# Kernel tuning notes

Hardware: AMD Instinct MI355X
Metric: run time of the kernel (lower is better)

## Reference

```python
import jax, jax.numpy as jnp
import numpy as np

IN_F, OUT_F, RANK, BLK = 4096, 4096, 64, 64
N_BLOCKS = min(IN_F, OUT_F) // BLK  # 64


def setup_inputs() -> dict:
    key = jax.random.key(0)
    ks = jax.random.split(key, 6)
    s = 0.02
    x = jax.random.normal(ks[0], (4, 2048, IN_F), dtype=jnp.float32)
    diag_params = jax.random.normal(ks[1], (N_BLOCKS, IN_F // N_BLOCKS, OUT_F // N_BLOCKS), dtype=jnp.float32) * s
    W_left = jax.random.normal(ks[2], (RANK, IN_F), dtype=jnp.float32) * s   # torch Linear weight [out,in]
    W_right = jax.random.normal(ks[3], (OUT_F, RANK), dtype=jnp.float32) * s
    b_right = jax.random.normal(ks[4], (OUT_F,), dtype=jnp.float32) * s
    bias = jax.random.normal(ks[5], (OUT_F,), dtype=jnp.float32) * s
    return {"x": x, "diag_params": diag_params, "W_left": W_left,
            "W_right": W_right, "b_right": b_right, "bias": bias}


def reference(x, diag_params, W_left, W_right, b_right, bias):
    nb, bi, bo = diag_params.shape
    lead = x.shape[:-1]
    # block-diagonal matmul: x @ block_diag(*diag_params), without materializing the dense matrix
    xb = x.reshape(*lead, nb, bi)                       # [..., nb, bi]
    x1 = jnp.einsum('...nd,ndo->...no', xb, diag_params).reshape(*lead, nb * bo)
    # low-rank path: right(left(x)) with right's bias
    x2 = (x @ W_left.T) @ W_right.T + b_right
    return x1 + x2 + bias
```

## Files before the change

### kernel.cpp

```cpp
#include <hip/hip_runtime.h>
#include <hip/hip_bf16.h>
#include <stdint.h>


#define M_TOT   8192
#define IN_F    4096
#define OUT_F   4096
#define RANK    64
#define NBLK    64

typedef __attribute__((ext_vector_type(8))) short  bf16x8;
typedef __attribute__((ext_vector_type(4))) float  floatx4;

#define WS_BIAS   0
#define WS_WL     16384
#define WS_BP     540672
#define WS_T      1589248

__device__ __forceinline__ unsigned short f2bf(float f) {
    union { float f; unsigned int u; } v; v.f = f;
    unsigned int u = v.u;
    u += 0x7fffu + ((u >> 16) & 1u);
    return (unsigned short)(u >> 16);
}

__global__ __launch_bounds__(256) void prep_kernel(
    const float* __restrict__ diag, const float* __restrict__ Wl,
    const float* __restrict__ Wr,   const float* __restrict__ br,
    const float* __restrict__ bias,
    float* __restrict__ bias_comb, unsigned short* __restrict__ wl_pack,
    unsigned short* __restrict__ bp_pack)
{
    int tid = blockIdx.x * blockDim.x + threadIdx.x;
    int nthr = gridDim.x * blockDim.x;

    for (int i = tid; i < OUT_F; i += nthr)
        bias_comb[i] = br[i] + bias[i];

    for (int i = tid; i < 64 * 4096; i += nthr) {
        int n = i >> 12, c = i & 4095;
        wl_pack[((size_t)(c >> 5) * 64 + n) * 32 + (c & 31)] = f2bf(Wl[i]);
    }

    for (int i = tid; i < 64 * 64 * 64; i += nthr) {
        int nb = i >> 12, k = (i >> 6) & 63, n = i & 63;
        bp_pack[(((size_t)nb * 4 + (k >> 5)) * 64 + n) * 32 + (k & 31)] = f2bf(diag[i]);
    }

    for (int i = tid; i < 64 * 64 * 64; i += nthr) {
        int nb = i >> 12, n = (i >> 6) & 63, r = i & 63;
        int kt = 64 + r;
        bp_pack[(((size_t)nb * 4 + (kt >> 5)) * 64 + n) * 32 + (kt & 31)] = f2bf(Wr[i]);
    }
}

__global__ __launch_bounds__(256) void k1_lowrank(
    const float* __restrict__ x, const unsigned short* __restrict__ wl_pack,
    float* __restrict__ t)
{
    int wave = blockIdx.x * 4 + (threadIdx.x >> 6);
    int lane = threadIdx.x & 63;
    int q = lane >> 4, l = lane & 15;
    int mt = wave >> 3;
    int ks = wave & 7;
    int m0 = mt * 16;
    int kc0 = ks * 16;

    const float* xrow = x + (size_t)(m0 + l) * IN_F + q * 8;
    floatx4 acc[4] = {};

    #pragma unroll 4
    for (int kc = kc0; kc < kc0 + 16; ++kc) {
        const float* ap = xrow + kc * 32;
        float4 a0 = *(const float4*)(ap);
        float4 a1 = *(const float4*)(ap + 4);
        bf16x8 af;
        af[0] = (short)f2bf(a0.x); af[1] = (short)f2bf(a0.y);
        af[2] = (short)f2bf(a0.z); af[3] = (short)f2bf(a0.w);
        af[4] = (short)f2bf(a1.x); af[5] = (short)f2bf(a1.y);
        af[6] = (short)f2bf(a1.z); af[7] = (short)f2bf(a1.w);
        #pragma unroll
        for (int nt = 0; nt < 4; ++nt) {
            bf16x8 bf = *(const bf16x8*)(wl_pack + ((size_t)(kc * 64 + nt * 16 + l) * 32 + q * 8));
            acc[nt] = __builtin_amdgcn_mfma_f32_16x16x32_bf16(af, bf, acc[nt], 0, 0, 0);
        }
    }

    #pragma unroll
    for (int nt = 0; nt < 4; ++nt)
        #pragma unroll
        for (int r = 0; r < 4; ++r)
            atomicAdd(&t[(size_t)(m0 + q * 4 + r) * RANK + nt * 16 + l], acc[nt][r]);
}

__global__ __launch_bounds__(256) void k2_out(
    const float* __restrict__ x, const unsigned short* __restrict__ bp_pack,
    const float* __restrict__ t, const float* __restrict__ bias_comb,
    float* __restrict__ out)
{
    int wave = blockIdx.x * 4 + (threadIdx.x >> 6);
    int lane = threadIdx.x & 63;
    int nb = wave >> 7;
    int mg = wave & 127;
    int q = lane >> 4, l = lane & 15;

    bf16x8 bfrag[4][4];
    #pragma unroll
    for (int kc = 0; kc < 4; ++kc)
        #pragma unroll
        for (int nt = 0; nt < 4; ++nt)
            bfrag[kc][nt] = *(const bf16x8*)(bp_pack +
                (((size_t)(nb * 4 + kc) * 64 + nt * 16 + l) * 32 + q * 8));

    float bval[4];
    #pragma unroll
    for (int nt = 0; nt < 4; ++nt)
        bval[nt] = bias_comb[nb * 64 + nt * 16 + l];

    float4 xa[8], xn[8];
    auto load_sub = [&](int sub, float4* dst) {
        int m0 = (mg * 4 + sub) * 16;
        const float* xp = x + (size_t)(m0 + l) * IN_F + nb * 64 + q * 8;
        dst[0] = *(const float4*)(xp);
        dst[1] = *(const float4*)(xp + 4);
        dst[2] = *(const float4*)(xp + 32);
        dst[3] = *(const float4*)(xp + 36);
        const float* tp = t + (size_t)(m0 + l) * RANK + q * 8;
        dst[4] = *(const float4*)(tp);
        dst[5] = *(const float4*)(tp + 4);
        dst[6] = *(const float4*)(tp + 32);
        dst[7] = *(const float4*)(tp + 36);
    };

    load_sub(0, xa);
    for (int sub = 0; sub < 4; ++sub) {
        if (sub < 3) load_sub(sub + 1, xn);

        bf16x8 afrag[4];
        #pragma unroll
        for (int kc = 0; kc < 4; ++kc) {
            float4 a0 = xa[kc * 2], a1 = xa[kc * 2 + 1];
            bf16x8 af;
            af[0] = (short)f2bf(a0.x); af[1] = (short)f2bf(a0.y);
            af[2] = (short)f2bf(a0.z); af[3] = (short)f2bf(a0.w);
            af[4] = (short)f2bf(a1.x); af[5] = (short)f2bf(a1.y);
            af[6] = (short)f2bf(a1.z); af[7] = (short)f2bf(a1.w);
            afrag[kc] = af;
        }

        floatx4 acc[4] = {};
        #pragma unroll
        for (int kc = 0; kc < 4; ++kc)
            #pragma unroll
            for (int nt = 0; nt < 4; ++nt)
                acc[nt] = __builtin_amdgcn_mfma_f32_16x16x32_bf16(afrag[kc], bfrag[kc][nt], acc[nt], 0, 0, 0);

        int m0 = (mg * 4 + sub) * 16;
        float* op = out + (size_t)m0 * OUT_F + nb * 64;
        #pragma unroll
        for (int nt = 0; nt < 4; ++nt)
            #pragma unroll
            for (int r = 0; r < 4; ++r)
                op[(size_t)(q * 4 + r) * OUT_F + nt * 16 + l] = acc[nt][r] + bval[nt];

        #pragma unroll
        for (int i = 0; i < 8; ++i) xa[i] = xn[i];
    }
}

extern "C" void kernel_launch(void* const* d_in, const int* in_sizes, int n_in,
                              void* d_out, int out_size, void* d_ws, size_t ws_size,
                              hipStream_t stream) {
    const float* x    = (const float*)d_in[0];
    const float* diag = (const float*)d_in[1];
    const float* Wl   = (const float*)d_in[2];
    const float* Wr   = (const float*)d_in[3];
    const float* br   = (const float*)d_in[4];
    const float* bias = (const float*)d_in[5];
    float* out = (float*)d_out;

    char* ws = (char*)d_ws;
    float*          bias_comb = (float*)(ws + WS_BIAS);
    unsigned short* wl_pack   = (unsigned short*)(ws + WS_WL);
    unsigned short* bp_pack   = (unsigned short*)(ws + WS_BP);
    float*          t         = (float*)(ws + WS_T);

    hipMemsetAsync(t, 0, (size_t)M_TOT * RANK * sizeof(float), stream);

    hipLaunchKernelGGL(prep_kernel, dim3(512), dim3(256), 0, stream,
                       diag, Wl, Wr, br, bias, bias_comb, wl_pack, bp_pack);
    hipLaunchKernelGGL(k1_lowrank, dim3(1024), dim3(256), 0, stream,
                       x, wl_pack, t);
    hipLaunchKernelGGL(k2_out, dim3(2048), dim3(256), 0, stream,
                       x, bp_pack, t, bias_comb, out);
}
```

Baseline: 315.4 us.

## Fuse low-rank projection and block-diagonal output into one kernel with LDS reduction

The low-rank x@W_left pass and the output pass are merged into a single kernel. Each block owns 16 rows, keeps the converted bf16 x fragments in registers (32 per wave), and reduces the four per-wave partial t values through shared memory instead of global atomics. This removes the memset, the atomics, the t round trip through global memory and the second read of x. The cost is heavy register pressure (xfrag[32] plus B fragments), only 512 blocks, and B fragments reloaded for each of the 16 block-diagonal tiles.

```diff
diff --git a/kernel.cpp b/kernel.cpp
--- a/kernel.cpp
+++ b/kernel.cpp
@@ -15,13 +15,23 @@
 #define WS_BIAS   0
 #define WS_WL     16384
 #define WS_BP     540672
-#define WS_T      1589248
+
+#define S_TP 68
 
 __device__ __forceinline__ unsigned short f2bf(float f) {
     union { float f; unsigned int u; } v; v.f = f;
     unsigned int u = v.u;
     u += 0x7fffu + ((u >> 16) & 1u);
     return (unsigned short)(u >> 16);
+}
+
+__device__ __forceinline__ bf16x8 cvt8(float4 a0, float4 a1) {
+    bf16x8 af;
+    af[0] = (short)f2bf(a0.x); af[1] = (short)f2bf(a0.y);
+    af[2] = (short)f2bf(a0.z); af[3] = (short)f2bf(a0.w);
+    af[4] = (short)f2bf(a1.x); af[5] = (short)f2bf(a1.y);
+    af[6] = (short)f2bf(a1.z); af[7] = (short)f2bf(a1.w);
+    return af;
 }
 
 __global__ __launch_bounds__(256) void prep_kernel(
@@ -54,35 +64,37 @@
     }
 }
 
-__global__ __launch_bounds__(256) void k1_lowrank(
+__global__ __launch_bounds__(256, 2) void fused_kernel(
     const float* __restrict__ x, const unsigned short* __restrict__ wl_pack,
-    float* __restrict__ t)
+    const unsigned short* __restrict__ bp_pack, const float* __restrict__ bias_comb,
+    float* __restrict__ out)
 {
-    int wave = blockIdx.x * 4 + (threadIdx.x >> 6);
+    __shared__ float t_part[4 * 16 * S_TP];
+
+    int w = threadIdx.x >> 6;
     int lane = threadIdx.x & 63;
     int q = lane >> 4, l = lane & 15;
-    int mt = wave >> 3;
-    int ks = wave & 7;
+    int mt = blockIdx.x;
     int m0 = mt * 16;
-    int kc0 = ks * 16;
+    int kc_g0 = w * 32;
 
     const float* xrow = x + (size_t)(m0 + l) * IN_F + q * 8;
-    floatx4 acc[4] = {};
 
-    #pragma unroll 4
-    for (int kc = kc0; kc < kc0 + 16; ++kc) {
-        const float* ap = xrow + kc * 32;
+    bf16x8 xfrag[32];
+    floatx4 tacc[4] = {};
+
+    #pragma unroll
+    for (int kc = 0; kc < 32; ++kc) {
+        int kc_g = kc_g0 + kc;
+        const float* ap = xrow + kc_g * 32;
         float4 a0 = *(const float4*)(ap);
         float4 a1 = *(const float4*)(ap + 4);
-        bf16x8 af;
-        af[0] = (short)f2bf(a0.x); af[1] = (short)f2bf(a0.y);
-        af[2] = (short)f2bf(a0.z); af[3] = (short)f2bf(a0.w);
-        af[4] = (short)f2bf(a1.x); af[5] = (short)f2bf(a1.y);
-        af[6] = (short)f2bf(a1.z); af[7] = (short)f2bf(a1.w);
+        bf16x8 af = cvt8(a0, a1);
+        xfrag[kc] = af;
         #pragma unroll
         for (int nt = 0; nt < 4; ++nt) {
-            bf16x8 bf = *(const bf16x8*)(wl_pack + ((size_t)(kc * 64 + nt * 16 + l) * 32 + q * 8));
-            acc[nt] = __builtin_amdgcn_mfma_f32_16x16x32_bf16(af, bf, acc[nt], 0, 0, 0);
+            bf16x8 bf = *(const bf16x8*)(wl_pack + ((size_t)(kc_g * 64 + nt * 16 + l) * 32 + q * 8));
+            tacc[nt] = __builtin_amdgcn_mfma_f32_16x16x32_bf16(af, bf, tacc[nt], 0, 0, 0);
         }
     }
 
@@ -90,81 +102,58 @@
     for (int nt = 0; nt < 4; ++nt)
         #pragma unroll
         for (int r = 0; r < 4; ++r)
-            atomicAdd(&t[(size_t)(m0 + q * 4 + r) * RANK + nt * 16 + l], acc[nt][r]);
-}
+            t_part[w * 16 * S_TP + (q * 4 + r) * S_TP + nt * 16 + l] = tacc[nt][r];
 
-__global__ __launch_bounds__(256) void k2_out(
-    const float* __restrict__ x, const unsigned short* __restrict__ bp_pack,
-    const float* __restrict__ t, const float* __restrict__ bias_comb,
-    float* __restrict__ out)
-{
-    int wave = blockIdx.x * 4 + (threadIdx.x >> 6);
-    int lane = threadIdx.x & 63;
-    int nb = wave >> 7;
-    int mg = wave & 127;
-    int q = lane >> 4, l = lane & 15;
+    __syncthreads();
 
-    bf16x8 bfrag[4][4];
+    bf16x8 tfrag[2];
     #pragma unroll
-    for (int kc = 0; kc < 4; ++kc)
+    for (int kc2 = 0; kc2 < 2; ++kc2) {
+        float4 s0 = {0.f, 0.f, 0.f, 0.f}, s1 = {0.f, 0.f, 0.f, 0.f};
         #pragma unroll
-        for (int nt = 0; nt < 4; ++nt)
-            bfrag[kc][nt] = *(const bf16x8*)(bp_pack +
-                (((size_t)(nb * 4 + kc) * 64 + nt * 16 + l) * 32 + q * 8));
+        for (int p = 0; p < 4; ++p) {
+            const float* tp = &t_part[p * 16 * S_TP + l * S_TP + kc2 * 32 + q * 8];
+            float4 v0 = *(const float4*)(tp);
+            float4 v1 = *(const float4*)(tp + 4);
+            s0.x += v0.x; s0.y += v0.y; s0.z += v0.z; s0.w += v0.w;
+            s1.x += v1.x; s1.y += v1.y; s1.z += v1.z; s1.w += v1.w;
+        }
+        tfrag[kc2] = cvt8(s0, s1);
+    }
 
-    float bval[4];
     #pragma unroll
-    for (int nt = 0; nt < 4; ++nt)
-        bval[nt] = bias_comb[nb * 64 + nt * 16 + l];
+    for (int i = 0; i < 16; ++i) {
+        int nb = w * 16 + i;
 
-    float4 xa[8], xn[8];
-    auto load_sub = [&](int sub, float4* dst) {
-        int m0 = (mg * 4 + sub) * 16;
-        const float* xp = x + (size_t)(m0 + l) * IN_F + nb * 64 + q * 8;
-        dst[0] = *(const float4*)(xp);
-        dst[1] = *(const float4*)(xp + 4);
-        dst[2] = *(const float4*)(xp + 32);
-        dst[3] = *(const float4*)(xp + 36);
-        const float* tp = t + (size_t)(m0 + l) * RANK + q * 8;
-        dst[4] = *(const float4*)(tp);
-        dst[5] = *(const float4*)(tp + 4);
-        dst[6] = *(const float4*)(tp + 32);
-        dst[7] = *(const float4*)(tp + 36);
-    };
-
-    load_sub(0, xa);
-    for (int sub = 0; sub < 4; ++sub) {
-        if (sub < 3) load_sub(sub + 1, xn);
-
-        bf16x8 afrag[4];
-        #pragma unroll
-        for (int kc = 0; kc < 4; ++kc) {
-            float4 a0 = xa[kc * 2], a1 = xa[kc * 2 + 1];
-            bf16x8 af;
-            af[0] = (short)f2bf(a0.x); af[1] = (short)f2bf(a0.y);
-            af[2] = (short)f2bf(a0.z); af[3] = (short)f2bf(a0.w);
-            af[4] = (short)f2bf(a1.x); af[5] = (short)f2bf(a1.y);
-            af[6] = (short)f2bf(a1.z); af[7] = (short)f2bf(a1.w);
-            afrag[kc] = af;
-        }
-
-        floatx4 acc[4] = {};
+        bf16x8 bfrag[4][4];
         #pragma unroll
         for (int kc = 0; kc < 4; ++kc)
             #pragma unroll
             for (int nt = 0; nt < 4; ++nt)
-                acc[nt] = __builtin_amdgcn_mfma_f32_16x16x32_bf16(afrag[kc], bfrag[kc][nt], acc[nt], 0, 0, 0);
+                bfrag[kc][nt] = *(const bf16x8*)(bp_pack +
+                    (((size_t)(nb * 4 + kc) * 64 + nt * 16 + l) * 32 + q * 8));
 
-        int m0 = (mg * 4 + sub) * 16;
+        floatx4 acc[4];
+        #pragma unroll
+        for (int nt = 0; nt < 4; ++nt) {
+            float bv = bias_comb[nb * 64 + nt * 16 + l];
+            acc[nt][0] = bv; acc[nt][1] = bv; acc[nt][2] = bv; acc[nt][3] = bv;
+        }
+
+        #pragma unroll
+        for (int kc = 0; kc < 4; ++kc) {
+            bf16x8 af = (kc < 2) ? xfrag[2 * i + kc] : tfrag[kc - 2];
+            #pragma unroll
+            for (int nt = 0; nt < 4; ++nt)
+                acc[nt] = __builtin_amdgcn_mfma_f32_16x16x32_bf16(af, bfrag[kc][nt], acc[nt], 0, 0, 0);
+        }
+
         float* op = out + (size_t)m0 * OUT_F + nb * 64;
         #pragma unroll
         for (int nt = 0; nt < 4; ++nt)
             #pragma unroll
             for (int r = 0; r < 4; ++r)
-                op[(size_t)(q * 4 + r) * OUT_F + nt * 16 + l] = acc[nt][r] + bval[nt];
-
-        #pragma unroll
-        for (int i = 0; i < 8; ++i) xa[i] = xn[i];
+                op[(size_t)(q * 4 + r) * OUT_F + nt * 16 + l] = acc[nt][r];
     }
 }
 
@@ -183,14 +172,9 @@
     float*          bias_comb = (float*)(ws + WS_BIAS);
     unsigned short* wl_pack   = (unsigned short*)(ws + WS_WL);
     unsigned short* bp_pack   = (unsigned short*)(ws + WS_BP);
-    float*          t         = (float*)(ws + WS_T);
-
-    hipMemsetAsync(t, 0, (size_t)M_TOT * RANK * sizeof(float), stream);
 
     hipLaunchKernelGGL(prep_kernel, dim3(512), dim3(256), 0, stream,
                        diag, Wl, Wr, br, bias, bias_comb, wl_pack, bp_pack);
-    hipLaunchKernelGGL(k1_lowrank, dim3(1024), dim3(256), 0, stream,
-                       x, wl_pack, t);
-    hipLaunchKernelGGL(k2_out, dim3(2048), dim3(256), 0, stream,
-                       x, bp_pack, t, bias_comb, out);
+    hipLaunchKernelGGL(fused_kernel, dim3(512), dim3(256), 0, stream,
+                       x, wl_pack, bp_pack, bias_comb, out);
 }
```

Result: faster. 308.2 us (-2.3%).
